# Optimization experiments

Hardware: AMD Instinct MI355X
Metric: run time of the kernel (lower is better)

The kernel has to match this reference:

```python
import jax, jax.numpy as jnp
import numpy as np

B, N, K, F, S = 128, 116, 4, 72, 8
TOPK = 10
INTRA_T, INTER_T = 0.1, 0.2


def _safe_corr(f):
    # f: [batch, d, m] -> corr [batch, d, d], matching torch _safe_compute_correlation
    c = f - f.mean(axis=2, keepdims=True)
    cov = jnp.einsum('bim,bjm->bij', c, c)
    var = jnp.diagonal(cov, axis1=1, axis2=2)
    std = jnp.sqrt(jnp.clip(var, 1e-8, None))[:, :, None]
    corr = cov / (std * std.transpose(0, 2, 1) + 1e-8)
    return jnp.clip(corr, -1.0, 1.0)


def _sym(m):
    return (m + m.swapaxes(-1, -2)) * 0.5


def setup_inputs():
    key = jax.random.key(0)
    ks = jax.random.split(key, 8)
    def lin(k, out_d, in_d):
        return jax.random.normal(k, (out_d, in_d), jnp.float32) * (1.0 / np.sqrt(in_d))
    return {
        'band_features': jax.random.normal(ks[0], (B, N, K, F), jnp.float32),
        'attn_weights': jax.random.uniform(ks[1], (B, N, S, K), jnp.float32),
        'intra_thresh_adj': jnp.zeros((), jnp.float32),
        'inter_thresh_adj': jnp.zeros((), jnp.float32),
        'attn_fuse_weight': jnp.asarray(0.5, jnp.float32),
        'intra_W1': lin(ks[2], 64, N), 'intra_b1': jnp.zeros((64,), jnp.float32),
        'intra_W2': lin(ks[3], N, 64), 'intra_b2': jnp.zeros((N,), jnp.float32),
        'inter_W1': lin(ks[4], 32, K), 'inter_b1': jnp.zeros((32,), jnp.float32),
        'inter_W2': lin(ks[5], K, 32), 'inter_b2': jnp.zeros((K,), jnp.float32),
        'comp_W': lin(ks[6], 128, 2 * F + 6), 'comp_b': jnp.zeros((128,), jnp.float32),
    }


def reference(band_features, attn_weights, intra_thresh_adj, inter_thresh_adj,
              attn_fuse_weight, intra_W1, intra_b1, intra_W2, intra_b2,
              inter_W1, inter_b1, inter_W2, inter_b2, comp_W, comp_b):
    dt = band_features.dtype
    # ---- intra-band graph: [B*K, N, N] correlations ----
    x = band_features.transpose(0, 2, 1, 3).reshape(B * K, N, F)
    corr = _safe_corr(x)
    th = INTRA_T + jax.nn.sigmoid(intra_thresh_adj) * 0.2
    tmask = (jnp.abs(corr) > th).astype(dt)
    _, idx = jax.lax.top_k(jnp.abs(corr), min(TOPK, N))  # [B*K, N, k]
    bix = jnp.arange(B * K)[:, None, None]
    rix = jnp.arange(N)[None, :, None]
    kmask = jnp.zeros_like(corr).at[bix, rix, idx].set(1.0)
    sc = jax.nn.relu(_sym(corr * tmask * kmask))
    h = jax.nn.relu(sc.reshape(-1, N) @ intra_W1.T + intra_b1)  # dropout = eval identity
    intra = jax.nn.sigmoid(h @ intra_W2.T + intra_b2).reshape(B * K, N, N)
    intra_adj = _sym(intra).reshape(B, K, N, N)
    # ---- inter-band graph: [B*N, K, K] correlations ----
    y = band_features.reshape(B * N, K, F)
    base = _safe_corr(y)
    a = attn_weights.reshape(B * N, S, K).transpose(0, 2, 1)  # [B*N, K, S]
    acorr = _safe_corr(a)
    fw = jax.nn.sigmoid(attn_fuse_weight)
    base = fw * base + (1.0 - fw) * acorr
    th2 = INTER_T + jax.nn.sigmoid(inter_thresh_adj) * 0.2
    sc2 = jax.nn.relu(_sym(base * (jnp.abs(base) > th2).astype(dt)))
    h2 = jax.nn.relu(sc2.reshape(-1, K) @ inter_W1.T + inter_b1)
    inter = jax.nn.sigmoid(h2 @ inter_W2.T + inter_b2).reshape(B * N, K, K)
    inter_adj = _sym(inter).reshape(B, N, K, K)
    # ---- unified graph assembly (vectorized replacement of nested loops) ----
    kk = jnp.arange(K)
    bd = jnp.zeros((B, K, N, K, N), dt).at[:, kk, :, kk, :].set(
        intra_adj.transpose(1, 0, 2, 3))  # block-diagonal intra blocks
    unified = bd.reshape(B, K * N, K * N)
    kk1, kk2, nn = np.meshgrid(np.arange(K), np.arange(K), np.arange(N), indexing='ij')
    sel = (kk1 != kk2).ravel()
    k1f, k2f, nf = kk1.ravel()[sel], kk2.ravel()[sel], nn.ravel()[sel]
    vals = inter_adj[:, nf, k1f, k2f]  # [B, M]
    unified_adj = unified.at[:, k1f * N + nf, k2f * N + nf].set(vals)
    # ---- node features ----
    node_features = band_features.transpose(0, 2, 1, 3).reshape(B, K * N, F)
    # ---- graph-level features ----
    node_mean = band_features.mean(axis=(1, 2))
    node_std = jnp.std(band_features, axis=(1, 2), ddof=1)  # torch unbiased std
    deg = (intra_adj > 0).astype(dt).sum(axis=3)  # [B, K, N]
    tri = jnp.einsum('bkij,bkji->bki', intra_adj, intra_adj)  # diag of A@A
    clus = tri / (deg ** 2 + 1e-8)
    dens = (inter_adj > 0).astype(dt).mean(axis=(2, 3))  # [B, N]
    stren = inter_adj.mean(axis=(2, 3))
    gf = jnp.concatenate([
        node_mean, node_std,
        deg.mean(axis=(1, 2))[:, None], jnp.std(deg, axis=(1, 2), ddof=1)[:, None],
        clus.mean(axis=(1, 2))[:, None], jnp.std(clus, axis=(1, 2), ddof=1)[:, None],
        dens.mean(axis=1)[:, None], stren.mean(axis=1)[:, None]], axis=1)
    graph_features = jax.nn.relu(gf @ comp_W.T + comp_b)
    # ---- sparsity scalars ----
    intra_sp = 1.0 - (intra_adj > 0).astype(dt).mean()
    inter_sp = 1.0 - (inter_adj > 0).astype(dt).mean()
    it, jt = float(B * K * N * N), float(B * N * K * K)
    total_sp = (intra_sp * it + inter_sp * jt) / (it + jt)
    return (unified_adj, node_features, graph_features, intra_adj, inter_adj,
            intra_sp, inter_sp, total_sp)
```

## Files before the change

### kernel.cpp

```cpp
#include <hip/hip_runtime.h>
#include <math.h>

#define NB 128
#define NN_ 116
#define NK 4
#define NF 72
#define NS 8
#define TOPK 10

#define BK (NB*NK)
#define BN (NB*NN_)
#define NN2 (NN_*NN_)
#define KN (NK*NN_)
#define ROWS (BK*NN_)
#define LROW 117

#define OFF_UNI 0
#define SZ_UNI (NB*KN*KN)
#define OFF_NF (OFF_UNI + SZ_UNI)
#define SZ_NF (NB*KN*NF)
#define OFF_GF (OFF_NF + SZ_NF)
#define SZ_GF (NB*128)
#define OFF_IA (OFF_GF + SZ_GF)
#define SZ_IA (NB*NK*NN_*NN_)
#define OFF_IE (OFF_IA + SZ_IA)
#define SZ_IE (NB*NN_*NK*NK)
#define OFF_SP (OFF_IE + SZ_IE)

#define SCR_SC 0
#define SCR_CORR (SCR_SC + SZ_IA)
#define SCR_DEG (SCR_CORR + SZ_IA)
#define SCR_CLUS (SCR_DEG + ROWS)
#define SCR_DENS (SCR_CLUS + ROWS)
#define SCR_STREN (SCR_DENS + BN)
#define SCR_AUX (SCR_STREN + BN)

__device__ __forceinline__ float sigmoidf_(float x){ return 1.0f/(1.0f+expf(-x)); }
__device__ __forceinline__ float dot4_(float4 a, float4 b){
    return fmaf(a.x,b.x, fmaf(a.y,b.y, fmaf(a.z,b.z, a.w*b.w)));
}
#define CLIP1(x) fminf(1.0f, fmaxf(-1.0f, (x)))

__global__ __launch_bounds__(256, 1) void k_corr(const float* __restrict__ band,
                                                 float* __restrict__ corr_out)
{
    __shared__ float sx[NF*120];
    __shared__ float smu[120], srs[120];
    int bk = blockIdx.x;
    int b = bk >> 2, k = bk & 3;
    int t = threadIdx.x;
    const float* xin = band + ((size_t)b*NN_*NK + k)*NF;
    for (int e = t; e < NN_*NF; e += 256){
        int n = e / NF, f = e - n*NF;
        sx[f*120 + n] = xin[(size_t)n*NK*NF + f];
    }
    for (int e = t; e < NF*4; e += 256)
        sx[(e>>2)*120 + NN_ + (e&3)] = 0.0f;
    __syncthreads();
    if (t < NN_){
        float s = 0.f, ss = 0.f;
        for (int f = 0; f < NF; ++f){ float v = sx[f*120+t]; s += v; ss += v*v; }
        float mu = s * (1.0f/NF);
        float sd = sqrtf(fmaxf(ss - s*mu, 1e-8f));
        smu[t] = mu; srs[t] = 1.0f/sd;
    }
    __syncthreads();
    for (int e = t; e < NF*NN_; e += 256){
        int f = e / NN_, n = e - f*NN_;
        sx[f*120+n] = (sx[f*120+n] - smu[n]) * srs[n];
    }
    __syncthreads();
    float* dst = corr_out + (size_t)bk * NN2;
    if (t < 225){
        int ti = t / 15, tj = t - ti*15;
        int i0 = ti*8, j0 = tj*8;
        float acc[8][8] = {};
        for (int f = 0; f < NF; ++f){
            const float4 a0 = *(const float4*)&sx[f*120 + i0];
            const float4 a1 = *(const float4*)&sx[f*120 + i0 + 4];
            const float4 c0 = *(const float4*)&sx[f*120 + j0];
            const float4 c1 = *(const float4*)&sx[f*120 + j0 + 4];
            float av[8] = {a0.x,a0.y,a0.z,a0.w,a1.x,a1.y,a1.z,a1.w};
            float cv[8] = {c0.x,c0.y,c0.z,c0.w,c1.x,c1.y,c1.z,c1.w};
            #pragma unroll
            for (int r = 0; r < 8; ++r)
                #pragma unroll
                for (int c = 0; c < 8; ++c)
                    acc[r][c] = fmaf(av[r], cv[c], acc[r][c]);
        }
        #pragma unroll
        for (int r = 0; r < 8; ++r){
            int i = i0 + r;
            if (i < NN_){
                float4 v0;
                v0.x = CLIP1(acc[r][0]); v0.y = CLIP1(acc[r][1]);
                v0.z = CLIP1(acc[r][2]); v0.w = CLIP1(acc[r][3]);
                *(float4*)&dst[i*NN_ + j0] = v0;
                if (j0 + 4 <= 112){
                    float4 v1;
                    v1.x = CLIP1(acc[r][4]); v1.y = CLIP1(acc[r][5]);
                    v1.z = CLIP1(acc[r][6]); v1.w = CLIP1(acc[r][7]);
                    *(float4*)&dst[i*NN_ + j0 + 4] = v1;
                }
            }
        }
    }
}

__global__ __launch_bounds__(256) void k_topk_mask(const float* __restrict__ corr_in,
    const float* __restrict__ thadj, float* __restrict__ sc_out)
{
    __shared__ float sc_[NN_*LROW];
    __shared__ unsigned skm[NN_*4];
    __shared__ unsigned stop[232*10];
    int bk = blockIdx.x;
    int t = threadIdx.x;
    const float* src = corr_in + (size_t)bk*NN2;
    for (int e = t; e < NN2; e += 256){
        int i = e / NN_, j = e - i*NN_;
        sc_[i*LROW + j] = src[e];
    }
    __syncthreads();
    if (t < 232){
        int r = t >> 1, h = t & 1;
        const float* row = &sc_[r*LROW + h*58];
        int jbase = h*58;
        unsigned tv[TOPK];
        #pragma unroll
        for (int p = 0; p < TOPK; ++p) tv[p] = 0u;
        for (int jj = 0; jj < 58; ++jj){
            float c = fabsf(row[jj]);
            unsigned u = (__float_as_uint(c) & 0xFFFFFF80u) | (unsigned)(127 - (jbase + jj));
            #pragma unroll
            for (int p = 0; p < TOPK; ++p){
                unsigned old = tv[p];
                bool gt = u > old;
                tv[p] = gt ? u : old;
                u = gt ? old : u;
            }
        }
        #pragma unroll
        for (int p = 0; p < TOPK; ++p) stop[t*10 + p] = tv[p];
    }
    __syncthreads();
    if (t < NN_){
        const unsigned* A = &stop[(2*t)*10];
        const unsigned* Bp = &stop[(2*t+1)*10];
        int pa = 0, pb = 0;
        unsigned m0=0,m1=0,m2=0,m3=0;
        #pragma unroll
        for (int p = 0; p < TOPK; ++p){
            unsigned ua = A[pa], ub = Bp[pb];
            unsigned u;
            if (ua > ub){ u = ua; ++pa; } else { u = ub; ++pb; }
            int j = 127 - (int)(u & 127u);
            unsigned bit = 1u << (j & 31);
            int w = j >> 5;
            if (w == 0) m0 |= bit; else if (w == 1) m1 |= bit; else if (w == 2) m2 |= bit; else m3 |= bit;
        }
        skm[t*4+0]=m0; skm[t*4+1]=m1; skm[t*4+2]=m2; skm[t*4+3]=m3;
    }
    __syncthreads();
    float th = 0.1f + sigmoidf_(thadj[0]) * 0.2f;
    float* dst = sc_out + (size_t)bk * NN2;
    for (int e = t; e < NN2; e += 256){
        int i = e / NN_, j = e - i*NN_;
        float cij = sc_[i*LROW + j];
        float cji = sc_[j*LROW + i];
        bool kij = (skm[i*4 + (j>>5)] >> (j&31)) & 1u;
        bool kji = (skm[j*4 + (i>>5)] >> (i&31)) & 1u;
        float mij = (fabsf(cij) > th && kij) ? cij : 0.0f;
        float mji = (fabsf(cji) > th && kji) ? cji : 0.0f;
        dst[e] = fmaxf(0.5f*(mij+mji), 0.0f);
    }
}

__global__ __launch_bounds__(256) void k_mlp(const float* __restrict__ sc,
    const float* __restrict__ W1, const float* __restrict__ b1,
    const float* __restrict__ W2, const float* __restrict__ b2,
    float* __restrict__ intra)
{
    __shared__ float sA_[14848];
    __shared__ float sH[64*68];
    __shared__ float sb1[64];
    __shared__ float sb2[128];
    int t = threadIdx.x;
    int r0 = blockIdx.x * 64;
    float* srow = sA_;
    float* sW1  = sA_ + 7424;
    for (int e4 = t; e4 < 1856; e4 += 256){
        *(float4*)&srow[e4*4] = *(const float4*)&sc[(size_t)r0*116 + e4*4];
        *(float4*)&sW1[e4*4]  = *(const float4*)&W1[e4*4];
    }
    if (t < 64) sb1[t] = b1[t];
    if (t < 128) sb2[t] = (t < NN_) ? b2[t] : 0.0f;
    __syncthreads();
    {
        int rg = t >> 4, og = t & 15;
        float acc[4][4] = {};
        for (int j4 = 0; j4 < 29; ++j4){
            float4 s[4], w[4];
            #pragma unroll
            for (int m = 0; m < 4; ++m) s[m] = *(const float4*)&srow[(rg+16*m)*116 + j4*4];
            #pragma unroll
            for (int n = 0; n < 4; ++n) w[n] = *(const float4*)&sW1[(og+16*n)*116 + j4*4];
            #pragma unroll
            for (int m = 0; m < 4; ++m)
                #pragma unroll
                for (int n = 0; n < 4; ++n)
                    acc[m][n] += dot4_(s[m], w[n]);
        }
        #pragma unroll
        for (int m = 0; m < 4; ++m)
            #pragma unroll
            for (int n = 0; n < 4; ++n)
                sH[(rg+16*m)*68 + og+16*n] = fmaxf(acc[m][n] + sb1[og+16*n], 0.0f);
    }
    __syncthreads();
    float* sW2 = sA_;
    for (int e = t; e < 128*64; e += 256){
        int j = e >> 6, o = e & 63;
        sW2[j*76 + o] = (j < NN_) ? W2[e] : 0.0f;
    }
    __syncthreads();
    {
        int rg = t >> 4, jg = t & 15;
        float acc[4][8] = {};
        for (int o4 = 0; o4 < 16; ++o4){
            float4 h[4], w[8];
            #pragma unroll
            for (int m = 0; m < 4; ++m) h[m] = *(const float4*)&sH[(rg+16*m)*68 + o4*4];
            #pragma unroll
            for (int q = 0; q < 8; ++q) w[q] = *(const float4*)&sW2[(jg+16*q)*76 + o4*4];
            #pragma unroll
            for (int m = 0; m < 4; ++m)
                #pragma unroll
                for (int q = 0; q < 8; ++q)
                    acc[m][q] += dot4_(h[m], w[q]);
        }
        #pragma unroll
        for (int m = 0; m < 4; ++m){
            int row = r0 + rg + 16*m;
            #pragma unroll
            for (int q = 0; q < 8; ++q){
                int j = jg + 16*q;
                if (j < NN_)
                    intra[(size_t)row*116 + j] = sigmoidf_(acc[m][q] + sb2[j]);
            }
        }
    }
}

__global__ __launch_bounds__(256) void k_sym_intra(const float* __restrict__ intra,
    float* __restrict__ intra_adj, float* __restrict__ deg_out, float* __restrict__ clus_out)
{
    __shared__ float sm[NN_*LROW];
    int bk = blockIdx.x, t = threadIdx.x;
    const float* src = intra + (size_t)bk*NN2;
    for (int e = t; e < NN2; e += 256){
        int i = e / NN_, j = e - i*NN_;
        sm[i*LROW + j] = src[e];
    }
    __syncthreads();
    float* dst = intra_adj + (size_t)bk*NN2;
    for (int e = t; e < NN2; e += 256){
        int i = e / NN_, j = e - i*NN_;
        dst[e] = 0.5f*(sm[i*LROW + j] + sm[j*LROW + i]);
    }
    if (t < NN_){
        float tri = 0.f; int dg = 0;
        for (int j = 0; j < NN_; ++j){
            float v = 0.5f*(sm[t*LROW+j] + sm[j*LROW+t]);
            tri = fmaf(v, v, tri);
            dg += (v > 0.f) ? 1 : 0;
        }
        float d = (float)dg;
        deg_out[(size_t)bk*NN_ + t] = d;
        clus_out[(size_t)bk*NN_ + t] = tri / (d*d + 1e-8f);
    }
}

__global__ __launch_bounds__(256) void k_inter(const float* __restrict__ band,
    const float* __restrict__ attn, const float* __restrict__ thadj2,
    const float* __restrict__ fwp,
    const float* __restrict__ W1, const float* __restrict__ b1,
    const float* __restrict__ W2, const float* __restrict__ b2,
    float* __restrict__ inter_out, float* __restrict__ dens_out, float* __restrict__ stren_out)
{
    __shared__ float sW1[128], sb1[32], sW2[128], sb2[4];
    __shared__ float sMat[256*4];
    int t = threadIdx.x;
    if (t < 128) sW1[t] = W1[t];
    if (t < 32) sb1[t] = b1[t];
    if (t >= 128 && t < 256) sW2[t-128] = W2[t-128];
    if (t < 4) sb2[t] = b2[t];
    __syncthreads();
    int l = t & 3;
    int il = t >> 2;
    size_t item = (size_t)blockIdx.x*64 + il;

    const float* xr = band + item*(NK*NF) + l*NF;
    float s=0,p0=0,p1=0,p2=0,p3=0;
    for (int f = 0; f < NF; ++f){
        float v = xr[f];
        float v1=__shfl_xor(v,1), v2=__shfl_xor(v,2), v3=__shfl_xor(v,3);
        s += v; p0=fmaf(v,v,p0); p1=fmaf(v,v1,p1); p2=fmaf(v,v2,p2); p3=fmaf(v,v3,p3);
    }
    float mu = s*(1.0f/NF);
    float mu1=__shfl_xor(mu,1), mu2=__shfl_xor(mu,2), mu3=__shfl_xor(mu,3);
    float sd = sqrtf(fmaxf(p0 - s*mu, 1e-8f));
    float sd1=__shfl_xor(sd,1), sd2=__shfl_xor(sd,2), sd3=__shfl_xor(sd,3);
    float c0 = CLIP1((p0 - (float)NF*mu*mu )/(sd*sd +1e-8f));
    float c1 = CLIP1((p1 - (float)NF*mu*mu1)/(sd*sd1+1e-8f));
    float c2 = CLIP1((p2 - (float)NF*mu*mu2)/(sd*sd2+1e-8f));
    float c3 = CLIP1((p3 - (float)NF*mu*mu3)/(sd*sd3+1e-8f));

    const float* ar = attn + item*(NS*NK) + l;
    float as=0,q0=0,q1=0,q2=0,q3=0;
    #pragma unroll
    for (int s8 = 0; s8 < NS; ++s8){
        float v = ar[s8*NK];
        float v1=__shfl_xor(v,1), v2=__shfl_xor(v,2), v3=__shfl_xor(v,3);
        as += v; q0=fmaf(v,v,q0); q1=fmaf(v,v1,q1); q2=fmaf(v,v2,q2); q3=fmaf(v,v3,q3);
    }
    float am = as*(1.0f/NS);
    float am1=__shfl_xor(am,1), am2=__shfl_xor(am,2), am3=__shfl_xor(am,3);
    float ad = sqrtf(fmaxf(q0 - as*am, 1e-8f));
    float ad1=__shfl_xor(ad,1), ad2=__shfl_xor(ad,2), ad3=__shfl_xor(ad,3);
    float a0 = CLIP1((q0 - (float)NS*am*am )/(ad*ad +1e-8f));
    float a1 = CLIP1((q1 - (float)NS*am*am1)/(ad*ad1+1e-8f));
    float a2 = CLIP1((q2 - (float)NS*am*am2)/(ad*ad2+1e-8f));
    float a3 = CLIP1((q3 - (float)NS*am*am3)/(ad*ad3+1e-8f));

    float fwv = sigmoidf_(fwp[0]);
    float g0 = fwv*c0 + (1.0f-fwv)*a0;
    float g1 = fwv*c1 + (1.0f-fwv)*a1;
    float g2 = fwv*c2 + (1.0f-fwv)*a2;
    float g3 = fwv*c3 + (1.0f-fwv)*a3;
    float th2 = 0.2f + sigmoidf_(thadj2[0])*0.2f;
    float m0 = (fabsf(g0)>th2)?g0:0.f;
    float m1 = (fabsf(g1)>th2)?g1:0.f;
    float m2 = (fabsf(g2)>th2)?g2:0.f;
    float m3 = (fabsf(g3)>th2)?g3:0.f;

    sMat[il*16 + l*4 + (l^0)] = m0;
    sMat[il*16 + l*4 + (l^1)] = m1;
    sMat[il*16 + l*4 + (l^2)] = m2;
    sMat[il*16 + l*4 + (l^3)] = m3;
    __syncthreads();
    float x0 = fmaxf(0.5f*(sMat[il*16 + l*4 + 0] + sMat[il*16 + 0*4 + l]), 0.f);
    float x1 = fmaxf(0.5f*(sMat[il*16 + l*4 + 1] + sMat[il*16 + 1*4 + l]), 0.f);
    float x2 = fmaxf(0.5f*(sMat[il*16 + l*4 + 2] + sMat[il*16 + 2*4 + l]), 0.f);
    float x3 = fmaxf(0.5f*(sMat[il*16 + l*4 + 3] + sMat[il*16 + 3*4 + l]), 0.f);

    float h[32];
    #pragma unroll
    for (int o = 0; o < 32; ++o){
        float acc = sb1[o];
        acc = fmaf(sW1[o*4+0], x0, acc);
        acc = fmaf(sW1[o*4+1], x1, acc);
        acc = fmaf(sW1[o*4+2], x2, acc);
        acc = fmaf(sW1[o*4+3], x3, acc);
        h[o] = fmaxf(acc, 0.f);
    }
    float o0=sb2[0], o1=sb2[1], o2=sb2[2], o3=sb2[3];
    #pragma unroll
    for (int o = 0; o < 32; ++o){
        float hv = h[o];
        o0 = fmaf(sW2[0*32+o], hv, o0);
        o1 = fmaf(sW2[1*32+o], hv, o1);
        o2 = fmaf(sW2[2*32+o], hv, o2);
        o3 = fmaf(sW2[3*32+o], hv, o3);
    }
    o0 = sigmoidf_(o0); o1 = sigmoidf_(o1); o2 = sigmoidf_(o2); o3 = sigmoidf_(o3);
    __syncthreads();
    sMat[il*16 + l*4 + 0] = o0;
    sMat[il*16 + l*4 + 1] = o1;
    sMat[il*16 + l*4 + 2] = o2;
    sMat[il*16 + l*4 + 3] = o3;
    __syncthreads();
    float y0 = 0.5f*(o0 + sMat[il*16 + 0*4 + l]);
    float y1 = 0.5f*(o1 + sMat[il*16 + 1*4 + l]);
    float y2 = 0.5f*(o2 + sMat[il*16 + 2*4 + l]);
    float y3 = 0.5f*(o3 + sMat[il*16 + 3*4 + l]);
    *(float4*)&inter_out[item*16 + l*4] = make_float4(y0,y1,y2,y3);

    float cnt = ((y0>0.f)?1.f:0.f) + ((y1>0.f)?1.f:0.f) + ((y2>0.f)?1.f:0.f) + ((y3>0.f)?1.f:0.f);
    float sum = y0+y1+y2+y3;
    cnt += __shfl_xor(cnt,1); cnt += __shfl_xor(cnt,2);
    sum += __shfl_xor(sum,1); sum += __shfl_xor(sum,2);
    if (l == 0){
        dens_out[item]  = cnt * (1.0f/16.0f);
        stren_out[item] = sum * (1.0f/16.0f);
    }
}

__global__ __launch_bounds__(256) void k_gstats_lin(const float* __restrict__ band,
    const float* __restrict__ deg, const float* __restrict__ clus,
    const float* __restrict__ dens, const float* __restrict__ stren,
    const float* __restrict__ Wc, const float* __restrict__ bc,
    float* __restrict__ gfo, float* __restrict__ aux)
{
    int b = blockIdx.x, t = threadIdx.x;
    __shared__ float sGf[152];
    __shared__ float sPs[18*14*4];
    __shared__ float sPq[18*14*4];
    __shared__ float sA[4], sB[4];

    if (t < 252){
        int fq = t % 18, g = t / 18;
        float4 s = make_float4(0,0,0,0), q = make_float4(0,0,0,0);
        const float* base = band + (size_t)b*(KN*NF);
        for (int nk = g; nk < KN; nk += 14){
            float4 v = *(const float4*)&base[nk*NF + fq*4];
            s.x += v.x; s.y += v.y; s.z += v.z; s.w += v.w;
            q.x = fmaf(v.x,v.x,q.x); q.y = fmaf(v.y,v.y,q.y);
            q.z = fmaf(v.z,v.z,q.z); q.w = fmaf(v.w,v.w,q.w);
        }
        int idx = (fq*14 + g)*4;
        *(float4*)&sPs[idx] = s;
        *(float4*)&sPq[idx] = q;
    }
    __syncthreads();
    if (t < NF){
        int fq = t >> 2, e = t & 3;
        float S = 0.f, Q = 0.f;
        for (int g = 0; g < 14; ++g){ S += sPs[(fq*14+g)*4+e]; Q += sPq[(fq*14+g)*4+e]; }
        float mean = S * (1.0f/(float)KN);
        float var = fmaxf((Q - S*mean)/((float)KN - 1.0f), 0.0f);
        sGf[t] = mean;
        sGf[NF + t] = sqrtf(var);
    }
    __syncthreads();

    float s = 0.f, ss = 0.f;
    for (int e = t; e < KN; e += 256){ float v = deg[(size_t)b*KN + e]; s += v; ss += v*v; }
    #pragma unroll
    for (int d = 1; d < 64; d <<= 1){ s += __shfl_xor(s,d); ss += __shfl_xor(ss,d); }
    if ((t & 63) == 0){ sA[t>>6] = s; sB[t>>6] = ss; }
    __syncthreads();
    if (t == 0){
        float S0 = sA[0]+sA[1]+sA[2]+sA[3], S1 = sB[0]+sB[1]+sB[2]+sB[3];
        float Mv = (float)KN, mean = S0/Mv;
        float var = fmaxf((S1 - S0*mean)/(Mv - 1.0f), 0.0f);
        sGf[144] = mean; sGf[145] = sqrtf(var);
        aux[b] = S0;
    }
    __syncthreads();

    s = 0.f; ss = 0.f;
    for (int e = t; e < KN; e += 256){ float v = clus[(size_t)b*KN + e]; s += v; ss += v*v; }
    #pragma unroll
    for (int d = 1; d < 64; d <<= 1){ s += __shfl_xor(s,d); ss += __shfl_xor(ss,d); }
    if ((t & 63) == 0){ sA[t>>6] = s; sB[t>>6] = ss; }
    __syncthreads();
    if (t == 0){
        float S0 = sA[0]+sA[1]+sA[2]+sA[3], S1 = sB[0]+sB[1]+sB[2]+sB[3];
        float Mv = (float)KN, mean = S0/Mv;
        float var = fmaxf((S1 - S0*mean)/(Mv - 1.0f), 0.0f);
        sGf[146] = mean; sGf[147] = sqrtf(var);
    }
    __syncthreads();

    s = 0.f; ss = 0.f;
    for (int e = t; e < NN_; e += 256){ s += dens[(size_t)b*NN_ + e]; ss += stren[(size_t)b*NN_ + e]; }
    #pragma unroll
    for (int d = 1; d < 64; d <<= 1){ s += __shfl_xor(s,d); ss += __shfl_xor(ss,d); }
    if ((t & 63) == 0){ sA[t>>6] = s; sB[t>>6] = ss; }
    __syncthreads();
    if (t == 0){
        float S0 = sA[0]+sA[1]+sA[2]+sA[3], S1 = sB[0]+sB[1]+sB[2]+sB[3];
        sGf[148] = S0 / (float)NN_;
        sGf[149] = S1 / (float)NN_;
        aux[128 + b] = S0 * 16.0f;
    }
    __syncthreads();

    if (t < 128){
        float acc = bc[t];
        const float* w = Wc + (size_t)t*150;
        for (int c = 0; c < 150; ++c) acc = fmaf(sGf[c], w[c], acc);
        gfo[(size_t)b*128 + t] = fmaxf(acc, 0.f);
    }
}

__global__ __launch_bounds__(128) void k_sparsity(const float* __restrict__ aux, float* __restrict__ out3)
{
    int t = threadIdx.x;
    float a = aux[t];
    float c = aux[128 + t];
    #pragma unroll
    for (int d = 1; d < 64; d <<= 1){ a += __shfl_xor(a,d); c += __shfl_xor(c,d); }
    __shared__ float sA[2], sC2[2];
    if ((t & 63) == 0){ sA[t>>6] = a; sC2[t>>6] = c; }
    __syncthreads();
    if (t == 0){
        float icnt = sA[0]+sA[1], jcnt = sC2[0]+sC2[1];
        const float it = 6889472.0f, jt = 237568.0f;
        float isp = 1.0f - icnt/it;
        float jsp = 1.0f - jcnt/jt;
        out3[0] = isp; out3[1] = jsp;
        out3[2] = (isp*it + jsp*jt)/(it + jt);
    }
}

__global__ __launch_bounds__(128) void k_uninf(const float* __restrict__ intra_adj,
    const float* __restrict__ inter_adj, const float* __restrict__ band,
    float* __restrict__ uni, float* __restrict__ nf)
{
    int row = blockIdx.x;
    int b = row / KN, p = row - b*KN;
    int k1 = p / NN_, i = p - k1*NN_;
    int t = threadIdx.x;
    if (t < NN_){
        int q0 = t*4;
        int k2 = t / 29;
        int j0 = q0 - k2*NN_;
        float4 v;
        if (k2 == k1){
            v = *(const float4*)&intra_adj[(((size_t)b*NK + k1)*NN_ + i)*NN_ + j0];
        } else {
            int d = i - j0;
            float val = 0.f;
            if (d >= 0 && d < 4)
                val = inter_adj[(((size_t)b*NN_ + i)*NK + k1)*NK + k2];
            v.x = (d==0)?val:0.f;
            v.y = (d==1)?val:0.f;
            v.z = (d==2)?val:0.f;
            v.w = (d==3)?val:0.f;
        }
        *(float4*)&uni[(size_t)row*KN + q0] = v;
    } else {
        for (int ff = t - NN_; ff < NF/4; ff += 12){
            float4 v = *(const float4*)&band[(((size_t)b*NN_ + i)*NK + k1)*NF + ff*4];
            *(float4*)&nf[((size_t)b*KN + p)*NF + ff*4] = v;
        }
    }
}

extern "C" void kernel_launch(void* const* d_in, const int* in_sizes, int n_in,
                              void* d_out, int out_size, void* d_ws, size_t ws_size,
                              hipStream_t stream)
{
    const float* band = (const float*)d_in[0];
    const float* attn = (const float*)d_in[1];
    const float* thA  = (const float*)d_in[2];
    const float* thE  = (const float*)d_in[3];
    const float* fw   = (const float*)d_in[4];
    const float* iW1  = (const float*)d_in[5];
    const float* ib1  = (const float*)d_in[6];
    const float* iW2  = (const float*)d_in[7];
    const float* ib2  = (const float*)d_in[8];
    const float* eW1  = (const float*)d_in[9];
    const float* eb1  = (const float*)d_in[10];
    const float* eW2  = (const float*)d_in[11];
    const float* eb2  = (const float*)d_in[12];
    const float* cW   = (const float*)d_in[13];
    const float* cb   = (const float*)d_in[14];

    float* out = (float*)d_out;
    float* uni = out + OFF_UNI;
    float* nf  = out + OFF_NF;
    float* gfo = out + OFF_GF;
    float* ia  = out + OFF_IA;
    float* ie  = out + OFF_IE;
    float* sp  = out + OFF_SP;

    float* scr_sc    = uni + SCR_SC;
    float* scr_corr  = uni + SCR_CORR;
    float* scr_deg   = uni + SCR_DEG;
    float* scr_clus  = uni + SCR_CLUS;
    float* scr_dens  = uni + SCR_DENS;
    float* scr_stren = uni + SCR_STREN;
    float* scr_aux   = uni + SCR_AUX;

    k_corr<<<BK, 256, 0, stream>>>(band, scr_corr);
    k_topk_mask<<<BK, 256, 0, stream>>>(scr_corr, thA, scr_sc);
    k_mlp<<<ROWS/64, 256, 0, stream>>>(scr_sc, iW1, ib1, iW2, ib2, scr_sc);
    k_sym_intra<<<BK, 256, 0, stream>>>(scr_sc, ia, scr_deg, scr_clus);
    k_inter<<<BN/64, 256, 0, stream>>>(band, attn, thE, fw, eW1, eb1, eW2, eb2,
                                       ie, scr_dens, scr_stren);
    k_gstats_lin<<<NB, 256, 0, stream>>>(band, scr_deg, scr_clus, scr_dens, scr_stren,
                                         cW, cb, gfo, scr_aux);
    k_sparsity<<<1, 128, 0, stream>>>(scr_aux, sp);
    k_uninf<<<NB*KN, 128, 0, stream>>>(ia, ie, band, uni, nf);
}
```

Measured before the change: 172.7 us.

## Fuse inter-band kernel into corr launch, widen topk/sym blocks, grid-stride uninf

Merges the inter-band graph computation into the correlation kernel as extra blocks, which removes one launch and lets the two independent stages run concurrently. Top-k and symmetrize kernels move to 512 threads, splitting each row four ways with a 4-way merge and shuffle reductions for degree and clustering. The unified-adjacency/node-feature copy becomes a flat grid-stride kernel with fully coalesced float4 writes. The corr blocks keep launch_bounds(256,1), so the fused kernel's occupancy limit also applies to the lightweight inter blocks.

```diff
diff --git a/kernel.cpp b/kernel.cpp
--- a/kernel.cpp
+++ b/kernel.cpp
@@ -41,94 +41,207 @@
 }
 #define CLIP1(x) fminf(1.0f, fmaxf(-1.0f, (x)))
 
-__global__ __launch_bounds__(256, 1) void k_corr(const float* __restrict__ band,
-                                                 float* __restrict__ corr_out)
+__global__ __launch_bounds__(256, 1) void k_corr_inter(const float* __restrict__ band,
+    const float* __restrict__ attn, const float* __restrict__ thadj2,
+    const float* __restrict__ fwp,
+    const float* __restrict__ eW1, const float* __restrict__ eb1,
+    const float* __restrict__ eW2, const float* __restrict__ eb2,
+    float* __restrict__ corr_out, float* __restrict__ inter_out,
+    float* __restrict__ dens_out, float* __restrict__ stren_out)
 {
     __shared__ float sx[NF*120];
     __shared__ float smu[120], srs[120];
-    int bk = blockIdx.x;
-    int b = bk >> 2, k = bk & 3;
+    __shared__ float sW1[128], sb1[32], sW2[128], sb2[4];
+    __shared__ float sMat[256*4];
     int t = threadIdx.x;
-    const float* xin = band + ((size_t)b*NN_*NK + k)*NF;
-    for (int e = t; e < NN_*NF; e += 256){
-        int n = e / NF, f = e - n*NF;
-        sx[f*120 + n] = xin[(size_t)n*NK*NF + f];
-    }
-    for (int e = t; e < NF*4; e += 256)
-        sx[(e>>2)*120 + NN_ + (e&3)] = 0.0f;
-    __syncthreads();
-    if (t < NN_){
-        float s = 0.f, ss = 0.f;
-        for (int f = 0; f < NF; ++f){ float v = sx[f*120+t]; s += v; ss += v*v; }
-        float mu = s * (1.0f/NF);
-        float sd = sqrtf(fmaxf(ss - s*mu, 1e-8f));
-        smu[t] = mu; srs[t] = 1.0f/sd;
-    }
-    __syncthreads();
-    for (int e = t; e < NF*NN_; e += 256){
-        int f = e / NN_, n = e - f*NN_;
-        sx[f*120+n] = (sx[f*120+n] - smu[n]) * srs[n];
-    }
-    __syncthreads();
-    float* dst = corr_out + (size_t)bk * NN2;
-    if (t < 225){
-        int ti = t / 15, tj = t - ti*15;
-        int i0 = ti*8, j0 = tj*8;
-        float acc[8][8] = {};
-        for (int f = 0; f < NF; ++f){
-            const float4 a0 = *(const float4*)&sx[f*120 + i0];
-            const float4 a1 = *(const float4*)&sx[f*120 + i0 + 4];
-            const float4 c0 = *(const float4*)&sx[f*120 + j0];
-            const float4 c1 = *(const float4*)&sx[f*120 + j0 + 4];
-            float av[8] = {a0.x,a0.y,a0.z,a0.w,a1.x,a1.y,a1.z,a1.w};
-            float cv[8] = {c0.x,c0.y,c0.z,c0.w,c1.x,c1.y,c1.z,c1.w};
-            #pragma unroll
-            for (int r = 0; r < 8; ++r)
+    if (blockIdx.x < 512){
+        int bk = blockIdx.x;
+        int b = bk >> 2, k = bk & 3;
+        const float* xin = band + ((size_t)b*NN_*NK + k)*NF;
+        for (int e = t; e < NN_*NF; e += 256){
+            int n = e / NF, f = e - n*NF;
+            sx[f*120 + n] = xin[(size_t)n*NK*NF + f];
+        }
+        for (int e = t; e < NF*4; e += 256)
+            sx[(e>>2)*120 + NN_ + (e&3)] = 0.0f;
+        __syncthreads();
+        if (t < NN_){
+            float s = 0.f, ss = 0.f;
+            for (int f = 0; f < NF; ++f){ float v = sx[f*120+t]; s += v; ss += v*v; }
+            float mu = s * (1.0f/NF);
+            float sd = sqrtf(fmaxf(ss - s*mu, 1e-8f));
+            smu[t] = mu; srs[t] = 1.0f/sd;
+        }
+        __syncthreads();
+        for (int e = t; e < NF*NN_; e += 256){
+            int f = e / NN_, n = e - f*NN_;
+            sx[f*120+n] = (sx[f*120+n] - smu[n]) * srs[n];
+        }
+        __syncthreads();
+        float* dst = corr_out + (size_t)bk * NN2;
+        if (t < 225){
+            int ti = t / 15, tj = t - ti*15;
+            int i0 = ti*8, j0 = tj*8;
+            float acc[8][8] = {};
+            for (int f = 0; f < NF; ++f){
+                const float4 a0 = *(const float4*)&sx[f*120 + i0];
+                const float4 a1 = *(const float4*)&sx[f*120 + i0 + 4];
+                const float4 c0 = *(const float4*)&sx[f*120 + j0];
+                const float4 c1 = *(const float4*)&sx[f*120 + j0 + 4];
+                float av[8] = {a0.x,a0.y,a0.z,a0.w,a1.x,a1.y,a1.z,a1.w};
+                float cv[8] = {c0.x,c0.y,c0.z,c0.w,c1.x,c1.y,c1.z,c1.w};
                 #pragma unroll
-                for (int c = 0; c < 8; ++c)
-                    acc[r][c] = fmaf(av[r], cv[c], acc[r][c]);
-        }
-        #pragma unroll
-        for (int r = 0; r < 8; ++r){
-            int i = i0 + r;
-            if (i < NN_){
-                float4 v0;
-                v0.x = CLIP1(acc[r][0]); v0.y = CLIP1(acc[r][1]);
-                v0.z = CLIP1(acc[r][2]); v0.w = CLIP1(acc[r][3]);
-                *(float4*)&dst[i*NN_ + j0] = v0;
-                if (j0 + 4 <= 112){
-                    float4 v1;
-                    v1.x = CLIP1(acc[r][4]); v1.y = CLIP1(acc[r][5]);
-                    v1.z = CLIP1(acc[r][6]); v1.w = CLIP1(acc[r][7]);
-                    *(float4*)&dst[i*NN_ + j0 + 4] = v1;
+                for (int r = 0; r < 8; ++r)
+                    #pragma unroll
+                    for (int c = 0; c < 8; ++c)
+                        acc[r][c] = fmaf(av[r], cv[c], acc[r][c]);
+            }
+            #pragma unroll
+            for (int r = 0; r < 8; ++r){
+                int i = i0 + r;
+                if (i < NN_){
+                    float4 v0;
+                    v0.x = CLIP1(acc[r][0]); v0.y = CLIP1(acc[r][1]);
+                    v0.z = CLIP1(acc[r][2]); v0.w = CLIP1(acc[r][3]);
+                    *(float4*)&dst[i*NN_ + j0] = v0;
+                    if (j0 + 4 <= 112){
+                        float4 v1;
+                        v1.x = CLIP1(acc[r][4]); v1.y = CLIP1(acc[r][5]);
+                        v1.z = CLIP1(acc[r][6]); v1.w = CLIP1(acc[r][7]);
+                        *(float4*)&dst[i*NN_ + j0 + 4] = v1;
+                    }
                 }
             }
         }
-    }
-}
-
-__global__ __launch_bounds__(256) void k_topk_mask(const float* __restrict__ corr_in,
+    } else {
+        if (t < 128) sW1[t] = eW1[t];
+        if (t < 32) sb1[t] = eb1[t];
+        if (t >= 128 && t < 256) sW2[t-128] = eW2[t-128];
+        if (t < 4) sb2[t] = eb2[t];
+        __syncthreads();
+        int l = t & 3;
+        int il = t >> 2;
+        size_t item = (size_t)(blockIdx.x - 512)*64 + il;
+
+        const float* xr = band + item*(NK*NF) + l*NF;
+        float s=0,p0=0,p1=0,p2=0,p3=0;
+        for (int f = 0; f < NF; ++f){
+            float v = xr[f];
+            float v1=__shfl_xor(v,1), v2=__shfl_xor(v,2), v3=__shfl_xor(v,3);
+            s += v; p0=fmaf(v,v,p0); p1=fmaf(v,v1,p1); p2=fmaf(v,v2,p2); p3=fmaf(v,v3,p3);
+        }
+        float mu = s*(1.0f/NF);
+        float mu1=__shfl_xor(mu,1), mu2=__shfl_xor(mu,2), mu3=__shfl_xor(mu,3);
+        float sd = sqrtf(fmaxf(p0 - s*mu, 1e-8f));
+        float sd1=__shfl_xor(sd,1), sd2=__shfl_xor(sd,2), sd3=__shfl_xor(sd,3);
+        float c0 = CLIP1((p0 - (float)NF*mu*mu )/(sd*sd +1e-8f));
+        float c1 = CLIP1((p1 - (float)NF*mu*mu1)/(sd*sd1+1e-8f));
+        float c2 = CLIP1((p2 - (float)NF*mu*mu2)/(sd*sd2+1e-8f));
+        float c3 = CLIP1((p3 - (float)NF*mu*mu3)/(sd*sd3+1e-8f));
+
+        const float* ar = attn + item*(NS*NK) + l;
+        float as=0,q0=0,q1=0,q2=0,q3=0;
+        #pragma unroll
+        for (int s8 = 0; s8 < NS; ++s8){
+            float v = ar[s8*NK];
+            float v1=__shfl_xor(v,1), v2=__shfl_xor(v,2), v3=__shfl_xor(v,3);
+            as += v; q0=fmaf(v,v,q0); q1=fmaf(v,v1,q1); q2=fmaf(v,v2,q2); q3=fmaf(v,v3,q3);
+        }
+        float am = as*(1.0f/NS);
+        float am1=__shfl_xor(am,1), am2=__shfl_xor(am,2), am3=__shfl_xor(am,3);
+        float ad = sqrtf(fmaxf(q0 - as*am, 1e-8f));
+        float ad1=__shfl_xor(ad,1), ad2=__shfl_xor(ad,2), ad3=__shfl_xor(ad,3);
+        float a0 = CLIP1((q0 - (float)NS*am*am )/(ad*ad +1e-8f));
+        float a1 = CLIP1((q1 - (float)NS*am*am1)/(ad*ad1+1e-8f));
+        float a2 = CLIP1((q2 - (float)NS*am*am2)/(ad*ad2+1e-8f));
+        float a3 = CLIP1((q3 - (float)NS*am*am3)/(ad*ad3+1e-8f));
+
+        float fwv = sigmoidf_(fwp[0]);
+        float g0 = fwv*c0 + (1.0f-fwv)*a0;
+        float g1 = fwv*c1 + (1.0f-fwv)*a1;
+        float g2 = fwv*c2 + (1.0f-fwv)*a2;
+        float g3 = fwv*c3 + (1.0f-fwv)*a3;
+        float th2 = 0.2f + sigmoidf_(thadj2[0])*0.2f;
+        float m0 = (fabsf(g0)>th2)?g0:0.f;
+        float m1 = (fabsf(g1)>th2)?g1:0.f;
+        float m2 = (fabsf(g2)>th2)?g2:0.f;
+        float m3 = (fabsf(g3)>th2)?g3:0.f;
+
+        sMat[il*16 + l*4 + (l^0)] = m0;
+        sMat[il*16 + l*4 + (l^1)] = m1;
+        sMat[il*16 + l*4 + (l^2)] = m2;
+        sMat[il*16 + l*4 + (l^3)] = m3;
+        __syncthreads();
+        float x0 = fmaxf(0.5f*(sMat[il*16 + l*4 + 0] + sMat[il*16 + 0*4 + l]), 0.f);
+        float x1 = fmaxf(0.5f*(sMat[il*16 + l*4 + 1] + sMat[il*16 + 1*4 + l]), 0.f);
+        float x2 = fmaxf(0.5f*(sMat[il*16 + l*4 + 2] + sMat[il*16 + 2*4 + l]), 0.f);
+        float x3 = fmaxf(0.5f*(sMat[il*16 + l*4 + 3] + sMat[il*16 + 3*4 + l]), 0.f);
+
+        float h[32];
+        #pragma unroll
+        for (int o = 0; o < 32; ++o){
+            float acc = sb1[o];
+            acc = fmaf(sW1[o*4+0], x0, acc);
+            acc = fmaf(sW1[o*4+1], x1, acc);
+            acc = fmaf(sW1[o*4+2], x2, acc);
+            acc = fmaf(sW1[o*4+3], x3, acc);
+            h[o] = fmaxf(acc, 0.f);
+        }
+        float o0=sb2[0], o1=sb2[1], o2=sb2[2], o3=sb2[3];
+        #pragma unroll
+        for (int o = 0; o < 32; ++o){
+            float hv = h[o];
+            o0 = fmaf(sW2[0*32+o], hv, o0);
+            o1 = fmaf(sW2[1*32+o], hv, o1);
+            o2 = fmaf(sW2[2*32+o], hv, o2);
+            o3 = fmaf(sW2[3*32+o], hv, o3);
+        }
+        o0 = sigmoidf_(o0); o1 = sigmoidf_(o1); o2 = sigmoidf_(o2); o3 = sigmoidf_(o3);
+        __syncthreads();
+        sMat[il*16 + l*4 + 0] = o0;
+        sMat[il*16 + l*4 + 1] = o1;
+        sMat[il*16 + l*4 + 2] = o2;
+        sMat[il*16 + l*4 + 3] = o3;
+        __syncthreads();
+        float y0 = 0.5f*(o0 + sMat[il*16 + 0*4 + l]);
+        float y1 = 0.5f*(o1 + sMat[il*16 + 1*4 + l]);
+        float y2 = 0.5f*(o2 + sMat[il*16 + 2*4 + l]);
+        float y3 = 0.5f*(o3 + sMat[il*16 + 3*4 + l]);
+        *(float4*)&inter_out[item*16 + l*4] = make_float4(y0,y1,y2,y3);
+
+        float cnt = ((y0>0.f)?1.f:0.f) + ((y1>0.f)?1.f:0.f) + ((y2>0.f)?1.f:0.f) + ((y3>0.f)?1.f:0.f);
+        float sum = y0+y1+y2+y3;
+        cnt += __shfl_xor(cnt,1); cnt += __shfl_xor(cnt,2);
+        sum += __shfl_xor(sum,1); sum += __shfl_xor(sum,2);
+        if (l == 0){
+            dens_out[item]  = cnt * (1.0f/16.0f);
+            stren_out[item] = sum * (1.0f/16.0f);
+        }
+    }
+}
+
+__global__ __launch_bounds__(512) void k_topk_mask(const float* __restrict__ corr_in,
     const float* __restrict__ thadj, float* __restrict__ sc_out)
 {
     __shared__ float sc_[NN_*LROW];
     __shared__ unsigned skm[NN_*4];
-    __shared__ unsigned stop[232*10];
+    __shared__ unsigned stop[464*10];
     int bk = blockIdx.x;
     int t = threadIdx.x;
     const float* src = corr_in + (size_t)bk*NN2;
-    for (int e = t; e < NN2; e += 256){
+    for (int e = t; e < NN2; e += 512){
         int i = e / NN_, j = e - i*NN_;
         sc_[i*LROW + j] = src[e];
     }
     __syncthreads();
-    if (t < 232){
-        int r = t >> 1, h = t & 1;
-        const float* row = &sc_[r*LROW + h*58];
-        int jbase = h*58;
+    if (t < NN_*4){
+        int r = t >> 2, q = t & 3;
+        const float* row = &sc_[r*LROW + q*29];
+        int jbase = q*29;
         unsigned tv[TOPK];
         #pragma unroll
         for (int p = 0; p < TOPK; ++p) tv[p] = 0u;
-        for (int jj = 0; jj < 58; ++jj){
+        for (int jj = 0; jj < 29; ++jj){
             float c = fabsf(row[jj]);
             unsigned u = (__float_as_uint(c) & 0xFFFFFF80u) | (unsigned)(127 - (jbase + jj));
             #pragma unroll
@@ -144,15 +257,19 @@
     }
     __syncthreads();
     if (t < NN_){
-        const unsigned* A = &stop[(2*t)*10];
-        const unsigned* Bp = &stop[(2*t+1)*10];
-        int pa = 0, pb = 0;
+        const unsigned* L0 = &stop[(4*t+0)*10];
+        const unsigned* L1 = &stop[(4*t+1)*10];
+        const unsigned* L2 = &stop[(4*t+2)*10];
+        const unsigned* L3 = &stop[(4*t+3)*10];
+        int i0=0, i1=0, i2=0, i3=0;
         unsigned m0=0,m1=0,m2=0,m3=0;
         #pragma unroll
         for (int p = 0; p < TOPK; ++p){
-            unsigned ua = A[pa], ub = Bp[pb];
-            unsigned u;
-            if (ua > ub){ u = ua; ++pa; } else { u = ub; ++pb; }
+            unsigned u0 = L0[i0], u1 = L1[i1], u2 = L2[i2], u3 = L3[i3];
+            unsigned ua = u0 > u1 ? u0 : u1;
+            unsigned ub = u2 > u3 ? u2 : u3;
+            unsigned u  = ua > ub ? ua : ub;
+            if (u == u0) ++i0; else if (u == u1) ++i1; else if (u == u2) ++i2; else ++i3;
             int j = 127 - (int)(u & 127u);
             unsigned bit = 1u << (j & 31);
             int w = j >> 5;
@@ -163,7 +280,7 @@
     __syncthreads();
     float th = 0.1f + sigmoidf_(thadj[0]) * 0.2f;
     float* dst = sc_out + (size_t)bk * NN2;
-    for (int e = t; e < NN2; e += 256){
+    for (int e = t; e < NN2; e += 512){
         int i = e / NN_, j = e - i*NN_;
         float cij = sc_[i*LROW + j];
         float cji = sc_[j*LROW + i];
@@ -251,147 +368,37 @@
     }
 }
 
-__global__ __launch_bounds__(256) void k_sym_intra(const float* __restrict__ intra,
+__global__ __launch_bounds__(512) void k_sym_intra(const float* __restrict__ intra,
     float* __restrict__ intra_adj, float* __restrict__ deg_out, float* __restrict__ clus_out)
 {
     __shared__ float sm[NN_*LROW];
     int bk = blockIdx.x, t = threadIdx.x;
     const float* src = intra + (size_t)bk*NN2;
-    for (int e = t; e < NN2; e += 256){
+    for (int e = t; e < NN2; e += 512){
         int i = e / NN_, j = e - i*NN_;
         sm[i*LROW + j] = src[e];
     }
     __syncthreads();
     float* dst = intra_adj + (size_t)bk*NN2;
-    for (int e = t; e < NN2; e += 256){
+    for (int e = t; e < NN2; e += 512){
         int i = e / NN_, j = e - i*NN_;
         dst[e] = 0.5f*(sm[i*LROW + j] + sm[j*LROW + i]);
     }
-    if (t < NN_){
-        float tri = 0.f; int dg = 0;
-        for (int j = 0; j < NN_; ++j){
-            float v = 0.5f*(sm[t*LROW+j] + sm[j*LROW+t]);
+    if (t < NN_*4){
+        int r = t >> 2, q = t & 3;
+        float tri = 0.f, dg = 0.f;
+        for (int jj = 0; jj < 29; ++jj){
+            int j = q*29 + jj;
+            float v = 0.5f*(sm[r*LROW+j] + sm[j*LROW+r]);
             tri = fmaf(v, v, tri);
-            dg += (v > 0.f) ? 1 : 0;
-        }
-        float d = (float)dg;
-        deg_out[(size_t)bk*NN_ + t] = d;
-        clus_out[(size_t)bk*NN_ + t] = tri / (d*d + 1e-8f);
-    }
-}
-
-__global__ __launch_bounds__(256) void k_inter(const float* __restrict__ band,
-    const float* __restrict__ attn, const float* __restrict__ thadj2,
-    const float* __restrict__ fwp,
-    const float* __restrict__ W1, const float* __restrict__ b1,
-    const float* __restrict__ W2, const float* __restrict__ b2,
-    float* __restrict__ inter_out, float* __restrict__ dens_out, float* __restrict__ stren_out)
-{
-    __shared__ float sW1[128], sb1[32], sW2[128], sb2[4];
-    __shared__ float sMat[256*4];
-    int t = threadIdx.x;
-    if (t < 128) sW1[t] = W1[t];
-    if (t < 32) sb1[t] = b1[t];
-    if (t >= 128 && t < 256) sW2[t-128] = W2[t-128];
-    if (t < 4) sb2[t] = b2[t];
-    __syncthreads();
-    int l = t & 3;
-    int il = t >> 2;
-    size_t item = (size_t)blockIdx.x*64 + il;
-
-    const float* xr = band + item*(NK*NF) + l*NF;
-    float s=0,p0=0,p1=0,p2=0,p3=0;
-    for (int f = 0; f < NF; ++f){
-        float v = xr[f];
-        float v1=__shfl_xor(v,1), v2=__shfl_xor(v,2), v3=__shfl_xor(v,3);
-        s += v; p0=fmaf(v,v,p0); p1=fmaf(v,v1,p1); p2=fmaf(v,v2,p2); p3=fmaf(v,v3,p3);
-    }
-    float mu = s*(1.0f/NF);
-    float mu1=__shfl_xor(mu,1), mu2=__shfl_xor(mu,2), mu3=__shfl_xor(mu,3);
-    float sd = sqrtf(fmaxf(p0 - s*mu, 1e-8f));
-    float sd1=__shfl_xor(sd,1), sd2=__shfl_xor(sd,2), sd3=__shfl_xor(sd,3);
-    float c0 = CLIP1((p0 - (float)NF*mu*mu )/(sd*sd +1e-8f));
-    float c1 = CLIP1((p1 - (float)NF*mu*mu1)/(sd*sd1+1e-8f));
-    float c2 = CLIP1((p2 - (float)NF*mu*mu2)/(sd*sd2+1e-8f));
-    float c3 = CLIP1((p3 - (float)NF*mu*mu3)/(sd*sd3+1e-8f));
-
-    const float* ar = attn + item*(NS*NK) + l;
-    float as=0,q0=0,q1=0,q2=0,q3=0;
-    #pragma unroll
-    for (int s8 = 0; s8 < NS; ++s8){
-        float v = ar[s8*NK];
-        float v1=__shfl_xor(v,1), v2=__shfl_xor(v,2), v3=__shfl_xor(v,3);
-        as += v; q0=fmaf(v,v,q0); q1=fmaf(v,v1,q1); q2=fmaf(v,v2,q2); q3=fmaf(v,v3,q3);
-    }
-    float am = as*(1.0f/NS);
-    float am1=__shfl_xor(am,1), am2=__shfl_xor(am,2), am3=__shfl_xor(am,3);
-    float ad = sqrtf(fmaxf(q0 - as*am, 1e-8f));
-    float ad1=__shfl_xor(ad,1), ad2=__shfl_xor(ad,2), ad3=__shfl_xor(ad,3);
-    float a0 = CLIP1((q0 - (float)NS*am*am )/(ad*ad +1e-8f));
-    float a1 = CLIP1((q1 - (float)NS*am*am1)/(ad*ad1+1e-8f));
-    float a2 = CLIP1((q2 - (float)NS*am*am2)/(ad*ad2+1e-8f));
-    float a3 = CLIP1((q3 - (float)NS*am*am3)/(ad*ad3+1e-8f));
-
-    float fwv = sigmoidf_(fwp[0]);
-    float g0 = fwv*c0 + (1.0f-fwv)*a0;
-    float g1 = fwv*c1 + (1.0f-fwv)*a1;
-    float g2 = fwv*c2 + (1.0f-fwv)*a2;
-    float g3 = fwv*c3 + (1.0f-fwv)*a3;
-    float th2 = 0.2f + sigmoidf_(thadj2[0])*0.2f;
-    float m0 = (fabsf(g0)>th2)?g0:0.f;
-    float m1 = (fabsf(g1)>th2)?g1:0.f;
-    float m2 = (fabsf(g2)>th2)?g2:0.f;
-    float m3 = (fabsf(g3)>th2)?g3:0.f;
-
-    sMat[il*16 + l*4 + (l^0)] = m0;
-    sMat[il*16 + l*4 + (l^1)] = m1;
-    sMat[il*16 + l*4 + (l^2)] = m2;
-    sMat[il*16 + l*4 + (l^3)] = m3;
-    __syncthreads();
-    float x0 = fmaxf(0.5f*(sMat[il*16 + l*4 + 0] + sMat[il*16 + 0*4 + l]), 0.f);
-    float x1 = fmaxf(0.5f*(sMat[il*16 + l*4 + 1] + sMat[il*16 + 1*4 + l]), 0.f);
-    float x2 = fmaxf(0.5f*(sMat[il*16 + l*4 + 2] + sMat[il*16 + 2*4 + l]), 0.f);
-    float x3 = fmaxf(0.5f*(sMat[il*16 + l*4 + 3] + sMat[il*16 + 3*4 + l]), 0.f);
-
-    float h[32];
-    #pragma unroll
-    for (int o = 0; o < 32; ++o){
-        float acc = sb1[o];
-        acc = fmaf(sW1[o*4+0], x0, acc);
-        acc = fmaf(sW1[o*4+1], x1, acc);
-        acc = fmaf(sW1[o*4+2], x2, acc);
-        acc = fmaf(sW1[o*4+3], x3, acc);
-        h[o] = fmaxf(acc, 0.f);
-    }
-    float o0=sb2[0], o1=sb2[1], o2=sb2[2], o3=sb2[3];
-    #pragma unroll
-    for (int o = 0; o < 32; ++o){
-        float hv = h[o];
-        o0 = fmaf(sW2[0*32+o], hv, o0);
-        o1 = fmaf(sW2[1*32+o], hv, o1);
-        o2 = fmaf(sW2[2*32+o], hv, o2);
-        o3 = fmaf(sW2[3*32+o], hv, o3);
-    }
-    o0 = sigmoidf_(o0); o1 = sigmoidf_(o1); o2 = sigmoidf_(o2); o3 = sigmoidf_(o3);
-    __syncthreads();
-    sMat[il*16 + l*4 + 0] = o0;
-    sMat[il*16 + l*4 + 1] = o1;
-    sMat[il*16 + l*4 + 2] = o2;
-    sMat[il*16 + l*4 + 3] = o3;
-    __syncthreads();
-    float y0 = 0.5f*(o0 + sMat[il*16 + 0*4 + l]);
-    float y1 = 0.5f*(o1 + sMat[il*16 + 1*4 + l]);
-    float y2 = 0.5f*(o2 + sMat[il*16 + 2*4 + l]);
-    float y3 = 0.5f*(o3 + sMat[il*16 + 3*4 + l]);
-    *(float4*)&inter_out[item*16 + l*4] = make_float4(y0,y1,y2,y3);
-
-    float cnt = ((y0>0.f)?1.f:0.f) + ((y1>0.f)?1.f:0.f) + ((y2>0.f)?1.f:0.f) + ((y3>0.f)?1.f:0.f);
-    float sum = y0+y1+y2+y3;
-    cnt += __shfl_xor(cnt,1); cnt += __shfl_xor(cnt,2);
-    sum += __shfl_xor(sum,1); sum += __shfl_xor(sum,2);
-    if (l == 0){
-        dens_out[item]  = cnt * (1.0f/16.0f);
-        stren_out[item] = sum * (1.0f/16.0f);
+            dg += (v > 0.f) ? 1.f : 0.f;
+        }
+        tri += __shfl_xor(tri,1); tri += __shfl_xor(tri,2);
+        dg  += __shfl_xor(dg,1);  dg  += __shfl_xor(dg,2);
+        if (q == 0){
+            deg_out[(size_t)bk*NN_ + r]  = dg;
+            clus_out[(size_t)bk*NN_ + r] = tri / (dg*dg + 1e-8f);
+        }
     }
 }
 
@@ -504,18 +511,23 @@
     }
 }
 
-__global__ __launch_bounds__(128) void k_uninf(const float* __restrict__ intra_adj,
+#define UNQ (SZ_UNI/4)
+#define NFQ (SZ_NF/4)
+__global__ __launch_bounds__(256) void k_uninf(const float* __restrict__ intra_adj,
     const float* __restrict__ inter_adj, const float* __restrict__ band,
     float* __restrict__ uni, float* __restrict__ nf)
 {
-    int row = blockIdx.x;
-    int b = row / KN, p = row - b*KN;
-    int k1 = p / NN_, i = p - k1*NN_;
-    int t = threadIdx.x;
-    if (t < NN_){
-        int q0 = t*4;
-        int k2 = t / 29;
-        int j0 = q0 - k2*NN_;
+    int gid = blockIdx.x*256 + threadIdx.x;
+    int gsz = gridDim.x*256;
+    for (int q = gid; q < UNQ; q += gsz){
+        int row = q / 116;
+        int cq  = q - row*116;
+        int b = row / KN;
+        int p = row - b*KN;
+        int k1 = p / NN_;
+        int i  = p - k1*NN_;
+        int k2 = cq / 29;
+        int j0 = cq*4 - k2*NN_;
         float4 v;
         if (k2 == k1){
             v = *(const float4*)&intra_adj[(((size_t)b*NK + k1)*NN_ + i)*NN_ + j0];
@@ -529,12 +541,17 @@
             v.z = (d==2)?val:0.f;
             v.w = (d==3)?val:0.f;
         }
-        *(float4*)&uni[(size_t)row*KN + q0] = v;
-    } else {
-        for (int ff = t - NN_; ff < NF/4; ff += 12){
-            float4 v = *(const float4*)&band[(((size_t)b*NN_ + i)*NK + k1)*NF + ff*4];
-            *(float4*)&nf[((size_t)b*KN + p)*NF + ff*4] = v;
-        }
+        *(float4*)&uni[(size_t)q*4] = v;
+    }
+    for (int q = gid; q < NFQ; q += gsz){
+        int fq = q % 18;
+        int rest = q / 18;
+        int b = rest / KN;
+        int p = rest - b*KN;
+        int k = p / NN_;
+        int n = p - k*NN_;
+        float4 v = *(const float4*)&band[(((size_t)b*NN_ + n)*NK + k)*NF + fq*4];
+        *(float4*)&nf[(size_t)q*4] = v;
     }
 }
 
@@ -574,14 +591,13 @@
     float* scr_stren = uni + SCR_STREN;
     float* scr_aux   = uni + SCR_AUX;
 
-    k_corr<<<BK, 256, 0, stream>>>(band, scr_corr);
-    k_topk_mask<<<BK, 256, 0, stream>>>(scr_corr, thA, scr_sc);
+    k_corr_inter<<<512 + BN/64, 256, 0, stream>>>(band, attn, thE, fw, eW1, eb1, eW2, eb2,
+                                                  scr_corr, ie, scr_dens, scr_stren);
+    k_topk_mask<<<BK, 512, 0, stream>>>(scr_corr, thA, scr_sc);
     k_mlp<<<ROWS/64, 256, 0, stream>>>(scr_sc, iW1, ib1, iW2, ib2, scr_sc);
-    k_sym_intra<<<BK, 256, 0, stream>>>(scr_sc, ia, scr_deg, scr_clus);
-    k_inter<<<BN/64, 256, 0, stream>>>(band, attn, thE, fw, eW1, eb1, eW2, eb2,
-                                       ie, scr_dens, scr_stren);
+    k_sym_intra<<<BK, 512, 0, stream>>>(scr_sc, ia, scr_deg, scr_clus);
     k_gstats_lin<<<NB, 256, 0, stream>>>(band, scr_deg, scr_clus, scr_dens, scr_stren,
                                          cW, cb, gfo, scr_aux);
     k_sparsity<<<1, 128, 0, stream>>>(scr_aux, sp);
-    k_uninf<<<NB*KN, 128, 0, stream>>>(ia, ie, band, uni, nf);
-}
+    k_uninf<<<2048, 256, 0, stream>>>(ia, ie, band, uni, nf);
+}
```

Measured after the change: 158.1 us. 1.09x faster.
